# Performance work log

Measured on AMD Instinct MI355X. Metric: run time of the kernel, lower is better.

Reference implementation:

```python
import jax, jax.numpy as jnp
import numpy as np

B, S, C, V = 8, 1024, 2048, 50257


def setup_inputs() -> dict:
    key = jax.random.key(0)
    kx, ky, kw, kb = jax.random.split(key, 4)
    x = jax.random.normal(kx, (B, S, C), dtype=jnp.float32)
    y = jax.random.randint(ky, (B, S), 0, V, dtype=jnp.int64)
    # nn.Linear default init: U(-1/sqrt(C), 1/sqrt(C))
    bound = 1.0 / np.sqrt(C)
    W = jax.random.uniform(kw, (V, C), dtype=jnp.float32, minval=-bound, maxval=bound)
    b = jax.random.uniform(kb, (V,), dtype=jnp.float32, minval=-bound, maxval=bound)
    return {"x": x, "y": y, "W": W, "b": b}


def reference(x, y, W, b):
    # logits: [N, V] where N = B*S
    xf = x.reshape(-1, x.shape[-1])
    yf = y.reshape(-1)
    logits = xf @ W.T + b
    logp = jax.nn.log_softmax(logits, axis=-1)
    nll = -jnp.take_along_axis(logp, yf[:, None], axis=-1)[:, 0]
    return jnp.mean(nll)
```

## Files before the change

kernel.cpp:

```cpp
#include <hip/hip_runtime.h>
#include <hip/hip_bf16.h>
#include <cstdint>

#define N_ROWS 8192
#define CDIM   2048
#define VDIM   50257
#define BM     128
#define BN     128
#define BK     32
#define VTILES 393
#define KT_ITERS (CDIM / BK)

static_assert(VTILES == (VDIM + BN - 1) / BN, "vtile count");

using short8 = __attribute__((ext_vector_type(8))) short;
using u16x8  = __attribute__((ext_vector_type(8))) unsigned short;
using f32x4  = __attribute__((ext_vector_type(4))) float;

__device__ __forceinline__ unsigned short f2bf(float f) {
    unsigned int u = __float_as_uint(f);
    u += 0x7FFFu + ((u >> 16) & 1u);
    return (unsigned short)(u >> 16);
}

__global__ __launch_bounds__(256) void cvt_bf16_kernel(const float* __restrict__ in,
                                                       unsigned short* __restrict__ out,
                                                       long n8) {
    long stride = (long)gridDim.x * blockDim.x;
    for (long i = (long)blockIdx.x * blockDim.x + threadIdx.x; i < n8; i += stride) {
        const float4* p = (const float4*)in + 2 * i;
        float4 a = p[0];
        float4 b = p[1];
        u16x8 v;
        v[0] = f2bf(a.x); v[1] = f2bf(a.y); v[2] = f2bf(a.z); v[3] = f2bf(a.w);
        v[4] = f2bf(b.x); v[5] = f2bf(b.y); v[6] = f2bf(b.z); v[7] = f2bf(b.w);
        ((u16x8*)out)[i] = v;
    }
}

__device__ __forceinline__ int slot_perm(int r) { return (r ^ (r >> 1)) & 3; }

__device__ __forceinline__ void gload_lds16(const void* g, void* l) {
    __builtin_amdgcn_global_load_lds(
        (const __attribute__((address_space(1))) unsigned int*)g,
        (__attribute__((address_space(3))) unsigned int*)l, 16, 0, 0);
}

__global__ __launch_bounds__(256) void gemm_lse_kernel(const unsigned short* __restrict__ Xb,
                                                       const unsigned short* __restrict__ Wb,
                                                       const float* __restrict__ bias,
                                                       float* __restrict__ partials) {
    int bid = blockIdx.x;
    int cpx = gridDim.x >> 3;
    int wg  = (bid & 7) * cpx + (bid >> 3);
    int rt  = wg & 63;
    int vt  = wg >> 6;
    int row0 = rt * BM;
    int v0   = vt * BN;

    __shared__ unsigned short Abuf[BM * BK];
    __shared__ unsigned short Bbuf[BN * BK];
    __shared__ float ps[2][BM];

    const int t  = threadIdx.x;
    const int w  = t >> 6;
    const int l  = t & 63;
    const int wr = w >> 1;
    const int wc = w & 1;
    const int g  = l >> 4;
    const int lr = l & 15;

    int sr[2], sk[2];
    #pragma unroll
    for (int i = 0; i < 2; ++i) {
        int c = t + i * 256;
        sr[i] = c >> 2;
        sk[i] = (c & 3) ^ slot_perm(c >> 2);
    }
    int bvrow[2];
    #pragma unroll
    for (int i = 0; i < 2; ++i) {
        int vr = v0 + sr[i];
        bvrow[i] = (vr < VDIM) ? vr : (VDIM - 1);
    }

    f32x4 acc[4][4];
    #pragma unroll
    for (int m = 0; m < 4; ++m)
        #pragma unroll
        for (int n = 0; n < 4; ++n)
            acc[m][n] = (f32x4)0.0f;

    const int arow_slot = slot_perm((wr * 64 + lr) & 15);

    for (int kt = 0; kt < KT_ITERS; ++kt) {
        const int k0 = kt * BK;
        #pragma unroll
        for (int i = 0; i < 2; ++i) {
            int c = t + i * 256;
            gload_lds16(Xb + (size_t)(row0 + sr[i]) * CDIM + k0 + sk[i] * 8,
                        &Abuf[c * 8]);
        }
        #pragma unroll
        for (int i = 0; i < 2; ++i) {
            int c = t + i * 256;
            gload_lds16(Wb + (size_t)bvrow[i] * CDIM + k0 + sk[i] * 8,
                        &Bbuf[c * 8]);
        }
        __syncthreads();

        short8 af[4], bfr[4];
        #pragma unroll
        for (int m = 0; m < 4; ++m) {
            int row = wr * 64 + m * 16 + lr;
            int sp  = g ^ slot_perm(row);
            af[m] = *(const short8*)&Abuf[row * BK + sp * 8];
        }
        #pragma unroll
        for (int n = 0; n < 4; ++n) {
            int row = wc * 64 + n * 16 + lr;
            int sp  = g ^ slot_perm(row);
            bfr[n] = *(const short8*)&Bbuf[row * BK + sp * 8];
        }
        #pragma unroll
        for (int m = 0; m < 4; ++m)
            #pragma unroll
            for (int n = 0; n < 4; ++n)
                acc[m][n] = __builtin_amdgcn_mfma_f32_16x16x32_bf16(
                    af[m], bfr[n], acc[m][n], 0, 0, 0);
        __syncthreads();
    }

    float bvals[4];
    bool  valid[4];
    #pragma unroll
    for (int n = 0; n < 4; ++n) {
        int v = v0 + wc * 64 + n * 16 + lr;
        valid[n] = (v < VDIM);
        bvals[n] = valid[n] ? bias[v] : 0.0f;
    }
    #pragma unroll
    for (int m = 0; m < 4; ++m) {
        #pragma unroll
        for (int i = 0; i < 4; ++i) {
            float s = 0.0f;
            #pragma unroll
            for (int n = 0; n < 4; ++n) {
                float e = valid[n] ? __expf(acc[m][n][i] + bvals[n]) : 0.0f;
                s += e;
            }
            s += __shfl_xor(s, 1);
            s += __shfl_xor(s, 2);
            s += __shfl_xor(s, 4);
            s += __shfl_xor(s, 8);
            if (lr == 0) ps[wc][wr * 64 + m * 16 + g * 4 + i] = s;
        }
    }
    __syncthreads();
    if (t < BM) {
        float s = ps[0][t] + ps[1][t];
        partials[(size_t)(row0 + t) * VTILES + vt] = s;
    }
}

__global__ __launch_bounds__(256) void tgt_kernel(const float* __restrict__ x,
                                                  const float* __restrict__ W,
                                                  const float* __restrict__ bias,
                                                  const int* __restrict__ y,
                                                  float* __restrict__ tgt) {
    int row = blockIdx.x * 4 + (threadIdx.x >> 6);
    int l   = threadIdx.x & 63;
    int yv  = y[row];
    const float4* xr = (const float4*)(x + (size_t)row * CDIM);
    const float4* wr = (const float4*)(W + (size_t)yv * CDIM);
    float s = 0.0f;
    #pragma unroll
    for (int i = l; i < CDIM / 4; i += 64) {
        float4 a = xr[i];
        float4 b = wr[i];
        s += a.x * b.x + a.y * b.y + a.z * b.z + a.w * b.w;
    }
    #pragma unroll
    for (int off = 32; off > 0; off >>= 1) s += __shfl_down(s, off);
    if (l == 0) tgt[row] = s + bias[yv];
}

__global__ __launch_bounds__(256) void reduce_kernel(const float* __restrict__ partials,
                                                     const float* __restrict__ tgt,
                                                     float* __restrict__ acc) {
    int row = blockIdx.x * 4 + (threadIdx.x >> 6);
    int l   = threadIdx.x & 63;
    const float* p = partials + (size_t)row * VTILES;
    float s = 0.0f;
    for (int i = l; i < VTILES; i += 64) s += p[i];
    #pragma unroll
    for (int off = 32; off > 0; off >>= 1) s += __shfl_down(s, off);
    if (l == 0) {
        float loss = logf(s) - tgt[row];
        atomicAdd(acc, loss);
    }
}

__global__ void finalize_kernel(const float* __restrict__ acc, float* __restrict__ out) {
    if (threadIdx.x == 0) out[0] = acc[0] * (1.0f / (float)N_ROWS);
}

extern "C" void kernel_launch(void* const* d_in, const int* in_sizes, int n_in,
                              void* d_out, int out_size, void* d_ws, size_t ws_size,
                              hipStream_t stream) {
    const float* x    = (const float*)d_in[0];
    const int*   y    = (const int*)d_in[1];
    const float* W    = (const float*)d_in[2];
    const float* bias = (const float*)d_in[3];
    float* out = (float*)d_out;

    const size_t W_BYTES = (size_t)VDIM * CDIM * 2;
    const size_t X_BYTES = (size_t)N_ROWS * CDIM * 2;
    const size_t P_BYTES = (size_t)N_ROWS * VTILES * 4;
    const size_t T_BYTES = (size_t)N_ROWS * 4;
    char* ws = (char*)d_ws;
    unsigned short* Wb = (unsigned short*)ws;
    unsigned short* Xb = (unsigned short*)(ws + W_BYTES);
    float* partials    = (float*)(ws + W_BYTES + X_BYTES);
    float* tgt         = (float*)(ws + W_BYTES + X_BYTES + P_BYTES);
    float* acc         = (float*)(ws + W_BYTES + X_BYTES + P_BYTES + T_BYTES);

    cvt_bf16_kernel<<<2048, 256, 0, stream>>>(W, Wb, (long)VDIM * CDIM / 8);
    cvt_bf16_kernel<<<2048, 256, 0, stream>>>(x, Xb, (long)N_ROWS * CDIM / 8);
    hipMemsetAsync(acc, 0, 4, stream);

    gemm_lse_kernel<<<64 * VTILES, 256, 0, stream>>>(Xb, Wb, bias, partials);
    tgt_kernel<<<N_ROWS / 4, 256, 0, stream>>>(x, W, bias, y, tgt);
    reduce_kernel<<<N_ROWS / 4, 256, 0, stream>>>(partials, tgt, acc);
    finalize_kernel<<<1, 64, 0, stream>>>(acc, out);
}
```

Before: 2.888 ms.

## Rewrite GEMM-LSE kernel with 256x256x64 tiles, double-buffered LDS and interleaved prefetch

Replaces the 128x128x32 single-buffered GEMM tile with a 256x256x64 tile processed by 8 waves, using double-buffered LDS and a new XOR swizzle. Global-to-LDS loads for the next k-tile are issued between four MFMA quadrant phases, with barriers and s_setprio to overlap memory with compute. The aim is to raise arithmetic intensity and hide load latency. In exchange it uses much more LDS and registers, and the hand-scheduled buffer indexing and waitcnt logic is fragile.

```diff
diff --git a/kernel.cpp b/kernel.cpp
--- a/kernel.cpp
+++ b/kernel.cpp
@@ -5,11 +5,11 @@
 #define N_ROWS 8192
 #define CDIM   2048
 #define VDIM   50257
-#define BM     128
-#define BN     128
-#define BK     32
-#define VTILES 393
-#define KT_ITERS (CDIM / BK)
+#define BM     256
+#define BN     256
+#define BK     64
+#define VTILES 197
+#define KTILES (CDIM / BK)
 
 static_assert(VTILES == (VDIM + BN - 1) / BN, "vtile count");
 
@@ -38,129 +38,207 @@
     }
 }
 
-__device__ __forceinline__ int slot_perm(int r) { return (r ^ (r >> 1)) & 3; }
-
 __device__ __forceinline__ void gload_lds16(const void* g, void* l) {
     __builtin_amdgcn_global_load_lds(
         (const __attribute__((address_space(1))) unsigned int*)g,
         (__attribute__((address_space(3))) unsigned int*)l, 16, 0, 0);
 }
 
-__global__ __launch_bounds__(256) void gemm_lse_kernel(const unsigned short* __restrict__ Xb,
-                                                       const unsigned short* __restrict__ Wb,
-                                                       const float* __restrict__ bias,
-                                                       float* __restrict__ partials) {
+__global__ __launch_bounds__(512, 2) void gemm_lse_kernel(const unsigned short* __restrict__ Xb,
+                                                          const unsigned short* __restrict__ Wb,
+                                                          const float* __restrict__ bias,
+                                                          float* __restrict__ partials) {
+    __shared__ unsigned short Alds[2][256][64];
+    __shared__ unsigned short Blds[2][256][64];
+    __shared__ float psm[4 * 256];
+
     int bid = blockIdx.x;
     int cpx = gridDim.x >> 3;
     int wg  = (bid & 7) * cpx + (bid >> 3);
-    int rt  = wg & 63;
-    int vt  = wg >> 6;
+    int rt  = wg & 31;
+    int vt  = wg >> 5;
     int row0 = rt * BM;
     int v0   = vt * BN;
 
-    __shared__ unsigned short Abuf[BM * BK];
-    __shared__ unsigned short Bbuf[BN * BK];
-    __shared__ float ps[2][BM];
-
     const int t  = threadIdx.x;
+    const int l  = t & 63;
     const int w  = t >> 6;
-    const int l  = t & 63;
-    const int wr = w >> 1;
-    const int wc = w & 1;
+    const int wr = w >> 2;
+    const int wc = w & 3;
     const int g  = l >> 4;
     const int lr = l & 15;
 
-    int sr[2], sk[2];
-    #pragma unroll
-    for (int i = 0; i < 2; ++i) {
-        int c = t + i * 256;
-        sr[i] = c >> 2;
-        sk[i] = (c & 3) ^ slot_perm(c >> 2);
-    }
-    int bvrow[2];
-    #pragma unroll
-    for (int i = 0; i < 2; ++i) {
-        int vr = v0 + sr[i];
-        bvrow[i] = (vr < VDIM) ? vr : (VDIM - 1);
-    }
-
-    f32x4 acc[4][4];
-    #pragma unroll
-    for (int m = 0; m < 4; ++m)
+    const int xorm  = (lr & 7) << 4;
+    const int colk0 = (g * 16) ^ xorm;
+    const int colk1 = (64 + g * 16) ^ xorm;
+    const int rbA   = wr * 16384 + lr * 128;
+    const int rbB   = wc * 8192  + lr * 128;
+
+    const int rl = t >> 3;
+    const int sl = (t & 7) ^ (rl & 7);
+    const unsigned short* pA00 = Xb + (size_t)(row0 +       rl     ) * CDIM + sl * 8;
+    const unsigned short* pA01 = Xb + (size_t)(row0 +       rl + 64) * CDIM + sl * 8;
+    const unsigned short* pA10 = Xb + (size_t)(row0 + 128 + rl     ) * CDIM + sl * 8;
+    const unsigned short* pA11 = Xb + (size_t)(row0 + 128 + rl + 64) * CDIM + sl * 8;
+    auto brow = [&](int r) -> size_t {
+        int v = v0 + r;
+        return (size_t)(v < VDIM ? v : VDIM - 1);
+    };
+    const unsigned short* pB00 = Wb + brow(      rl     ) * CDIM + sl * 8;
+    const unsigned short* pB01 = Wb + brow(      rl + 64) * CDIM + sl * 8;
+    const unsigned short* pB10 = Wb + brow(128 + rl     ) * CDIM + sl * 8;
+    const unsigned short* pB11 = Wb + brow(128 + rl + 64) * CDIM + sl * 8;
+
+    char* AlBase = (char*)&Alds[0][0][0];
+    char* BlBase = (char*)&Blds[0][0][0];
+    const int dst0 = t * 16;
+
+#define STAGE2(P0, P1, DB) do { \
+        gload_lds16((P0), (DB) + dst0); \
+        gload_lds16((P1), (DB) + dst0 + 8192); \
+    } while (0)
+
+    STAGE2(pA00, pA01, AlBase);
+    STAGE2(pA10, pA11, AlBase + 16384);
+    STAGE2(pB00, pB01, BlBase);
+    STAGE2(pB10, pB11, BlBase + 16384);
+    STAGE2(pB00 + 64, pB01 + 64, BlBase + 32768);
+    STAGE2(pB10 + 64, pB11 + 64, BlBase + 32768 + 16384);
+    pA00 += 64;  pA01 += 64;  pA10 += 64;  pA11 += 64;
+    pB00 += 128; pB01 += 128; pB10 += 128; pB11 += 128;
+    asm volatile("s_waitcnt vmcnt(4)" ::: "memory");
+    __builtin_amdgcn_s_barrier();
+
+    f32x4 acc[8][4];
+    #pragma unroll
+    for (int m = 0; m < 8; ++m)
         #pragma unroll
         for (int n = 0; n < 4; ++n)
             acc[m][n] = (f32x4)0.0f;
 
-    const int arow_slot = slot_perm((wr * 64 + lr) & 15);
-
-    for (int kt = 0; kt < KT_ITERS; ++kt) {
-        const int k0 = kt * BK;
-        #pragma unroll
-        for (int i = 0; i < 2; ++i) {
-            int c = t + i * 256;
-            gload_lds16(Xb + (size_t)(row0 + sr[i]) * CDIM + k0 + sk[i] * 8,
-                        &Abuf[c * 8]);
+    short8 af[2][4], bf[2][4];
+
+    for (int kt = 0; kt < KTILES; ++kt) {
+        const char* Ab = AlBase + (kt & 1) * 32768;
+        const char* Bb = BlBase + (kt & 1) * 32768;
+        char* An = AlBase + ((kt + 1) & 1) * 32768;
+        char* Bn = BlBase + (kt & 1) * 32768;
+
+        #pragma unroll
+        for (int ks = 0; ks < 2; ++ks) {
+            const int ck = ks ? colk1 : colk0;
+            #pragma unroll
+            for (int mm = 0; mm < 4; ++mm)
+                af[ks][mm] = *(const short8*)(Ab + rbA + mm * 2048 + ck);
+            #pragma unroll
+            for (int nn = 0; nn < 2; ++nn)
+                bf[ks][nn] = *(const short8*)(Bb + rbB + nn * 2048 + ck);
         }
-        #pragma unroll
-        for (int i = 0; i < 2; ++i) {
-            int c = t + i * 256;
-            gload_lds16(Wb + (size_t)bvrow[i] * CDIM + k0 + sk[i] * 8,
-                        &Bbuf[c * 8]);
+        STAGE2(pA00, pA01, An);
+        __builtin_amdgcn_s_barrier();
+        __builtin_amdgcn_s_setprio(1);
+        #pragma unroll
+        for (int ks = 0; ks < 2; ++ks)
+            #pragma unroll
+            for (int mm = 0; mm < 4; ++mm)
+                #pragma unroll
+                for (int nn = 0; nn < 2; ++nn)
+                    acc[mm][nn] = __builtin_amdgcn_mfma_f32_16x16x32_bf16(
+                        af[ks][mm], bf[ks][nn], acc[mm][nn], 0, 0, 0);
+        __builtin_amdgcn_s_setprio(0);
+        __builtin_amdgcn_s_barrier();
+
+        #pragma unroll
+        for (int ks = 0; ks < 2; ++ks) {
+            const int ck = ks ? colk1 : colk0;
+            #pragma unroll
+            for (int nn = 0; nn < 2; ++nn)
+                bf[ks][2 + nn] = *(const short8*)(Bb + rbB + (2 + nn) * 2048 + ck);
         }
-        __syncthreads();
-
-        short8 af[4], bfr[4];
-        #pragma unroll
-        for (int m = 0; m < 4; ++m) {
-            int row = wr * 64 + m * 16 + lr;
-            int sp  = g ^ slot_perm(row);
-            af[m] = *(const short8*)&Abuf[row * BK + sp * 8];
+        STAGE2(pA10, pA11, An + 16384);
+        __builtin_amdgcn_s_barrier();
+        __builtin_amdgcn_s_setprio(1);
+        #pragma unroll
+        for (int ks = 0; ks < 2; ++ks)
+            #pragma unroll
+            for (int mm = 0; mm < 4; ++mm)
+                #pragma unroll
+                for (int nn = 0; nn < 2; ++nn)
+                    acc[mm][2 + nn] = __builtin_amdgcn_mfma_f32_16x16x32_bf16(
+                        af[ks][mm], bf[ks][2 + nn], acc[mm][2 + nn], 0, 0, 0);
+        __builtin_amdgcn_s_setprio(0);
+        __builtin_amdgcn_s_barrier();
+
+        #pragma unroll
+        for (int ks = 0; ks < 2; ++ks) {
+            const int ck = ks ? colk1 : colk0;
+            #pragma unroll
+            for (int mm = 0; mm < 4; ++mm)
+                af[ks][mm] = *(const short8*)(Ab + rbA + 8192 + mm * 2048 + ck);
         }
-        #pragma unroll
-        for (int n = 0; n < 4; ++n) {
-            int row = wc * 64 + n * 16 + lr;
-            int sp  = g ^ slot_perm(row);
-            bfr[n] = *(const short8*)&Bbuf[row * BK + sp * 8];
-        }
-        #pragma unroll
-        for (int m = 0; m < 4; ++m)
-            #pragma unroll
-            for (int n = 0; n < 4; ++n)
-                acc[m][n] = __builtin_amdgcn_mfma_f32_16x16x32_bf16(
-                    af[m], bfr[n], acc[m][n], 0, 0, 0);
-        __syncthreads();
-    }
+        STAGE2(pB00, pB01, Bn);
+        __builtin_amdgcn_s_barrier();
+        __builtin_amdgcn_s_setprio(1);
+        #pragma unroll
+        for (int ks = 0; ks < 2; ++ks)
+            #pragma unroll
+            for (int mm = 0; mm < 4; ++mm)
+                #pragma unroll
+                for (int nn = 0; nn < 2; ++nn)
+                    acc[4 + mm][2 + nn] = __builtin_amdgcn_mfma_f32_16x16x32_bf16(
+                        af[ks][mm], bf[ks][2 + nn], acc[4 + mm][2 + nn], 0, 0, 0);
+        __builtin_amdgcn_s_setprio(0);
+        __builtin_amdgcn_s_barrier();
+
+        STAGE2(pB10, pB11, Bn + 16384);
+        __builtin_amdgcn_s_barrier();
+        __builtin_amdgcn_s_setprio(1);
+        #pragma unroll
+        for (int ks = 0; ks < 2; ++ks)
+            #pragma unroll
+            for (int mm = 0; mm < 4; ++mm)
+                #pragma unroll
+                for (int nn = 0; nn < 2; ++nn)
+                    acc[4 + mm][nn] = __builtin_amdgcn_mfma_f32_16x16x32_bf16(
+                        af[ks][mm], bf[ks][nn], acc[4 + mm][nn], 0, 0, 0);
+        __builtin_amdgcn_s_setprio(0);
+        pA00 += 64; pA01 += 64; pA10 += 64; pA11 += 64;
+        pB00 += 64; pB01 += 64; pB10 += 64; pB11 += 64;
+        asm volatile("s_waitcnt vmcnt(4)" ::: "memory");
+        __builtin_amdgcn_s_barrier();
+    }
+
+    asm volatile("s_waitcnt vmcnt(0)" ::: "memory");
 
     float bvals[4];
     bool  valid[4];
     #pragma unroll
-    for (int n = 0; n < 4; ++n) {
-        int v = v0 + wc * 64 + n * 16 + lr;
-        valid[n] = (v < VDIM);
-        bvals[n] = valid[n] ? bias[v] : 0.0f;
-    }
-    #pragma unroll
-    for (int m = 0; m < 4; ++m) {
+    for (int nn = 0; nn < 4; ++nn) {
+        int v = v0 + wc * 64 + nn * 16 + lr;
+        valid[nn] = (v < VDIM);
+        bvals[nn] = bias[valid[nn] ? v : 0];
+    }
+    #pragma unroll
+    for (int mm = 0; mm < 8; ++mm) {
         #pragma unroll
         for (int i = 0; i < 4; ++i) {
             float s = 0.0f;
             #pragma unroll
-            for (int n = 0; n < 4; ++n) {
-                float e = valid[n] ? __expf(acc[m][n][i] + bvals[n]) : 0.0f;
-                s += e;
-            }
+            for (int nn = 0; nn < 4; ++nn)
+                s += valid[nn] ? __expf(acc[mm][nn][i] + bvals[nn]) : 0.0f;
             s += __shfl_xor(s, 1);
             s += __shfl_xor(s, 2);
             s += __shfl_xor(s, 4);
             s += __shfl_xor(s, 8);
-            if (lr == 0) ps[wc][wr * 64 + m * 16 + g * 4 + i] = s;
+            if (lr == 0) psm[wc * 256 + wr * 128 + mm * 16 + g * 4 + i] = s;
         }
     }
     __syncthreads();
-    if (t < BM) {
-        float s = ps[0][t] + ps[1][t];
+    if (t < 256) {
+        float s = psm[t] + psm[256 + t] + psm[512 + t] + psm[768 + t];
         partials[(size_t)(row0 + t) * VTILES + vt] = s;
     }
+#undef STAGE2
 }
 
 __global__ __launch_bounds__(256) void tgt_kernel(const float* __restrict__ x,
@@ -225,11 +303,11 @@
     float* tgt         = (float*)(ws + W_BYTES + X_BYTES + P_BYTES);
     float* acc         = (float*)(ws + W_BYTES + X_BYTES + P_BYTES + T_BYTES);
 
-    cvt_bf16_kernel<<<2048, 256, 0, stream>>>(W, Wb, (long)VDIM * CDIM / 8);
+    cvt_bf16_kernel<<<4096, 256, 0, stream>>>(W, Wb, (long)VDIM * CDIM / 8);
     cvt_bf16_kernel<<<2048, 256, 0, stream>>>(x, Xb, (long)N_ROWS * CDIM / 8);
     hipMemsetAsync(acc, 0, 4, stream);
 
-    gemm_lse_kernel<<<64 * VTILES, 256, 0, stream>>>(Xb, Wb, bias, partials);
+    gemm_lse_kernel<<<32 * VTILES, 512, 0, stream>>>(Xb, Wb, bias, partials);
     tgt_kernel<<<N_ROWS / 4, 256, 0, stream>>>(x, W, bias, y, tgt);
     reduce_kernel<<<N_ROWS / 4, 256, 0, stream>>>(partials, tgt, acc);
     finalize_kernel<<<1, 64, 0, stream>>>(acc, out);
```

Measured after the change: 2.805 ms. -2.9%, faster.
